# Optimization experiments

Measured on AMD Instinct MI355X. Metric: run time of the kernel, lower is better.

## Reference

```python
import jax, jax.numpy as jnp
import numpy as np

N = 4_000_000   # number of sparse voxels
H = 128         # parent-grid extent per axis (input coords < 256 -> parents < 128)


def setup_inputs() -> dict:
    key = jax.random.key(0)
    # col 0 = batch index, cols 1:4 = integer xyz voxel coords in [0, 256)
    coords = jax.random.randint(key, (N, 4), 0, 256, dtype=jnp.int32)
    # spnn.Conv3d(1,1,k=2) kernel: (2^3, in=1, out=1), constant-init to 1.0
    kernel = jnp.ones((8, 1, 1), dtype=jnp.float32)
    return {"coords": coords, "kernel": kernel}


def _fog(coords, kernel):
    b = coords[:, 0].astype(jnp.int64)
    xyz = coords[:, 1:]
    # pos(): 3-bit occupancy code from LSBs of xyz, feat = 2^code
    bits = xyz & 1                                        # (N, 3)
    pos = bits[:, 0] + 2 * bits[:, 1] + 4 * bits[:, 2]    # (N,) in [0, 8)
    feats = (jnp.int32(1) << pos).astype(jnp.float32)     # (N,) values {1,...,128}

    # 2x2x2 stride-2 sparse conv with all-ones kernel == sum over the 8 children
    # of each parent voxel. The child's kernel-offset index is exactly `pos`.
    pxyz = (xyz >> 1).astype(jnp.int64)                   # parent coords
    pkey = ((b * H + pxyz[:, 0]) * H + pxyz[:, 1]) * H + pxyz[:, 2]

    ukeys, inv = jnp.unique(pkey, size=N, fill_value=-1, return_inverse=True)
    inv = inv.ravel()

    contrib = feats * kernel[pos, 0, 0]                   # all-ones kernel -> feats
    out_feats = jax.ops.segment_sum(contrib, inv, num_segments=N)  # (N,)

    # decode unique parent keys back to (batch, x, y, z); pad slots -> -1
    valid = ukeys >= 0
    k = jnp.where(valid, ukeys, 0)
    oz = k % H
    k = k // H
    oy = k % H
    k = k // H
    ox = k % H
    ob = k // H
    out_coords = jnp.stack([ob, ox, oy, oz], axis=-1).astype(jnp.int32)
    out_coords = jnp.where(valid[:, None], out_coords, jnp.int32(-1))
    return out_coords, out_feats


def reference(coords, kernel):
    return _fog(coords, kernel)
```

## Files before the change

kernel.cpp:

```cpp
#include <hip/hip_runtime.h>

#define NB_BITS     11
#define N_BUCKETS   (1 << NB_BITS)
#define LOCAL_BITS  18
#define LOCAL_WORDS 8192
#define LKMASK      ((1u << LOCAL_BITS) - 1u)
#define KEYMASK     0x1FFFFFFFu
#define NBLK        256
#define N_PART      8
#define FE_CAP      2560

__device__ __forceinline__ unsigned make_key(int4 c) {
    return ((((unsigned)c.x << 7) | (unsigned)(c.y >> 1)) << 7 | (unsigned)(c.z >> 1)) << 7
         | (unsigned)(c.w >> 1);
}

template<int NW>
__device__ inline void block_scan(unsigned v, unsigned* wsum, unsigned& excl, unsigned& total) {
    int t = threadIdx.x, ln = t & 63, wv = t >> 6;
    unsigned incl = v;
    #pragma unroll
    for (int off = 1; off < 64; off <<= 1) {
        unsigned y = __shfl_up(incl, off, 64);
        if (ln >= off) incl += y;
    }
    if (ln == 63) wsum[wv] = incl;
    __syncthreads();
    if (wv == 0) {
        unsigned s = (ln < NW) ? wsum[ln] : 0u;
        #pragma unroll
        for (int off = 1; off < NW; off <<= 1) {
            unsigned y = __shfl_up(s, off, 64);
            if (ln >= off) s += y;
        }
        if (ln < NW) wsum[ln] = s;
    }
    __syncthreads();
    excl = (wv ? wsum[wv - 1] : 0u) + incl - v;
    total = wsum[NW - 1];
}

__global__ void __launch_bounds__(1024)
hist_pass(const int4* __restrict__ coords,
          unsigned* __restrict__ hist32,
          unsigned* __restrict__ skeys, int n, int chunk) {
    __shared__ unsigned h[N_BUCKETS];
    int k = blockIdx.x, t = threadIdx.x;
    if (t < N_BUCKETS) h[t] = 0u;
    if (t + 1024 < N_BUCKETS) h[t + 1024] = 0u;
    __syncthreads();
    int s = k * chunk, e = min(n, s + chunk);
    for (int i = s + t; i < e; i += 1024) {
        int4 c = coords[i];
        unsigned key = make_key(c);
        unsigned pos = (unsigned)((c.y & 1) | ((c.z & 1) << 1) | ((c.w & 1) << 2));
        skeys[i] = (pos << 29) | key;
        atomicAdd(&h[key >> LOCAL_BITS], 1u);
    }
    __syncthreads();
    if (t < N_BUCKETS / 2)
        hist32[k * (N_BUCKETS / 2) + t] = h[2 * t] | (h[2 * t + 1] << 16);
}

__global__ void offs_pass(const unsigned* __restrict__ hist32,
                          unsigned* __restrict__ offs32,
                          unsigned* __restrict__ total) {
    int gid = blockIdx.x * blockDim.x + threadIdx.x;
    unsigned r0 = 0, r1 = 0;
    #pragma unroll 1
    for (int g = 0; g < N_PART; ++g)
        for (int j = 0; j < NBLK / N_PART; ++j) {
            int kk = j * N_PART + g;
            unsigned h = hist32[kk * (N_BUCKETS / 2) + gid];
            offs32[kk * (N_BUCKETS / 2) + gid] = r0 | (r1 << 16);
            r0 += h & 0xFFFFu; r1 += h >> 16;
        }
    total[2 * gid] = r0;
    total[2 * gid + 1] = r1;
}

__global__ void __launch_bounds__(1024)
scatter_pass(const unsigned* __restrict__ skeys,
             const unsigned* __restrict__ offs32,
             const unsigned* __restrict__ total,
             unsigned* __restrict__ pbase,
             unsigned* __restrict__ pairs, int n, int chunk) {
    __shared__ unsigned buf[N_BUCKETS];
    __shared__ unsigned wsum[16];
    int t = threadIdx.x, k = blockIdx.x;
    unsigned v0 = (t < N_BUCKETS / 2) ? total[2 * t] : 0u;
    unsigned v1 = (t < N_BUCKETS / 2) ? total[2 * t + 1] : 0u;
    unsigned excl, tot;
    block_scan<16>(v0 + v1, wsum, excl, tot);
    if (t < N_BUCKETS / 2) {
        unsigned o = offs32[k * (N_BUCKETS / 2) + t];
        buf[2 * t]     = excl + (o & 0xFFFFu);
        buf[2 * t + 1] = excl + v0 + (o >> 16);
        if (k == 0) {
            pbase[2 * t] = excl;
            pbase[2 * t + 1] = excl + v0;
            if (t == N_BUCKETS / 2 - 1) pbase[N_BUCKETS] = excl + v0 + v1;
        }
    }
    __syncthreads();
    int s = k * chunk, e = min(n, s + chunk);
    for (int i = s + t; i < e; i += 1024) {
        unsigned pk = skeys[i];
        unsigned b = (pk & KEYMASK) >> LOCAL_BITS;
        unsigned j = atomicAdd(&buf[b], 1u);
        pairs[j] = pk;
    }
}

__global__ void __launch_bounds__(1024, 2)
count_pass(const unsigned* __restrict__ pairs,
           const unsigned* __restrict__ pbase,
           unsigned* __restrict__ ucount) {
    __shared__ unsigned bm[LOCAL_WORDS];
    __shared__ unsigned wsum[16];
    int t = threadIdx.x, b = blockIdx.x;
    ((uint4*)bm)[t] = make_uint4(0u, 0u, 0u, 0u);
    ((uint4*)bm)[t + 1024] = make_uint4(0u, 0u, 0u, 0u);
    __syncthreads();
    unsigned s = pbase[b], e = pbase[b + 1];
    for (unsigned i = s + t; i < e; i += 1024) {
        unsigned lk = pairs[i] & LKMASK;
        atomicOr(&bm[lk >> 5], 1u << (lk & 31u));
    }
    __syncthreads();
    unsigned v = 0;
    #pragma unroll
    for (int m = 0; m < 8; ++m) v += __popc(bm[t + 1024 * m]);
    int ln = t & 63, wv = t >> 6;
    #pragma unroll
    for (int off = 1; off < 64; off <<= 1) v += __shfl_xor(v, off, 64);
    if (ln == 0) wsum[wv] = v;
    __syncthreads();
    if (t == 0) {
        unsigned c = 0;
        #pragma unroll
        for (int m = 0; m < 16; ++m) c += wsum[m];
        ucount[b] = c;
    }
}

__global__ void __launch_bounds__(1024, 2)
emit_pass(const unsigned* __restrict__ pairs,
          const unsigned* __restrict__ pbase,
          const unsigned* __restrict__ ucount,
          const float* __restrict__ kern,
          float4* __restrict__ out_coords,
          float* __restrict__ out_feats, int n) {
    __shared__ unsigned       bm[LOCAL_WORDS];
    __shared__ unsigned short pfx[LOCAL_WORDS];
    __shared__ float          fe[FE_CAP];
    __shared__ unsigned wsum[16];
    __shared__ unsigned ubS, totS;
    __shared__ float    kl[8];
    int t = threadIdx.x, b = blockIdx.x;
    if (t < 8) kl[t] = (float)(1 << t) * kern[t];
    ((uint4*)bm)[t] = make_uint4(0u, 0u, 0u, 0u);
    ((uint4*)bm)[t + 1024] = make_uint4(0u, 0u, 0u, 0u);
    for (int i = t; i < FE_CAP; i += 1024) fe[i] = 0.f;
    __syncthreads();
    unsigned s = pbase[b], e = pbase[b + 1];
    if (t < 64) {
        int ln = t;
        unsigned sum = 0;
        const uint4* uc4 = (const uint4*)ucount;
        #pragma unroll
        for (int q = 0; q < 8; ++q) {
            uint4 u = uc4[ln * 8 + q];
            sum += u.x + u.y + u.z + u.w;
        }
        unsigned incl = sum;
        #pragma unroll
        for (int off = 1; off < 64; off <<= 1) {
            unsigned y = __shfl_up(incl, off, 64);
            if (ln >= off) incl += y;
        }
        if (ln == 63) totS = incl;
        unsigned exclv = incl - sum;
        if (ln == (b >> 5)) {
            unsigned r = exclv;
            int lim = b & 31;
            for (int m = 0; m < lim; ++m) r += ucount[(b & ~31) + m];
            ubS = r;
        }
    } else {
        for (unsigned i = s + (unsigned)(t - 64); i < e; i += 960) {
            unsigned lk = pairs[i] & LKMASK;
            atomicOr(&bm[lk >> 5], 1u << (lk & 31u));
        }
    }
    __syncthreads();
    uint4 q0 = ((uint4*)bm)[2 * t], q1 = ((uint4*)bm)[2 * t + 1];
    unsigned pc[8] = { (unsigned)__popc(q0.x), (unsigned)__popc(q0.y),
                       (unsigned)__popc(q0.z), (unsigned)__popc(q0.w),
                       (unsigned)__popc(q1.x), (unsigned)__popc(q1.y),
                       (unsigned)__popc(q1.z), (unsigned)__popc(q1.w) };
    unsigned psum = 0;
    #pragma unroll
    for (int m = 0; m < 8; ++m) psum += pc[m];
    unsigned excl, cnt;
    block_scan<16>(psum, wsum, excl, cnt);
    unsigned run = excl;
    #pragma unroll
    for (int m = 0; m < 8; ++m) { pfx[8 * t + m] = (unsigned short)run; run += pc[m]; }
    __syncthreads();
    unsigned ub = ubS;
    for (unsigned i = s + t; i < e; i += 1024) {
        unsigned pk = pairs[i];
        unsigned key = pk & KEYMASK;
        unsigned lk = key & LKMASK;
        unsigned wd = lk >> 5;
        unsigned lr = (unsigned)pfx[wd] + __popc(bm[wd] & ((1u << (lk & 31u)) - 1u));
        atomicAdd(&fe[lr], kl[pk >> 29]);
        out_coords[ub + lr] = make_float4((float)(key >> 21),
                                          (float)((key >> 14) & 127u),
                                          (float)((key >> 7) & 127u),
                                          (float)(key & 127u));
    }
    __syncthreads();
    for (unsigned i = t; i < cnt; i += 1024)
        out_feats[ub + i] = fe[i];
    for (unsigned r = totS + (unsigned)(b * 1024 + t); r < (unsigned)n; r += N_BUCKETS * 1024u) {
        out_coords[r] = make_float4(-1.f, -1.f, -1.f, -1.f);
        out_feats[r] = 0.f;
    }
}

extern "C" void kernel_launch(void* const* d_in, const int* in_sizes, int n_in,
                              void* d_out, int out_size, void* d_ws, size_t ws_size,
                              hipStream_t stream) {
    const int4* coords = (const int4*)d_in[0];
    const float* kern  = (const float*)d_in[1];
    int N = in_sizes[0] / 4;

    float* out = (float*)d_out;
    float4* out_coords = (float4*)out;
    float* out_feats = out + (size_t)4 * N;

    unsigned* pairs  = (unsigned*)d_ws;
    unsigned* skeys  = pairs + (size_t)N;
    unsigned* hist32 = skeys + (size_t)N;
    unsigned* offs32 = hist32 + (size_t)NBLK * (N_BUCKETS / 2);
    unsigned* total  = offs32 + (size_t)NBLK * (N_BUCKETS / 2);
    unsigned* pbase  = total + N_BUCKETS;
    unsigned* ucount = pbase + 2064;

    int chunk = (N + NBLK - 1) / NBLK;
    hist_pass<<<NBLK, 1024, 0, stream>>>(coords, hist32, skeys, N, chunk);
    offs_pass<<<4, 256, 0, stream>>>(hist32, offs32, total);
    scatter_pass<<<NBLK, 1024, 0, stream>>>(skeys, offs32, total, pbase, pairs, N, chunk);
    count_pass<<<N_BUCKETS, 1024, 0, stream>>>(pairs, pbase, ucount);
    emit_pass<<<N_BUCKETS, 1024, 0, stream>>>(pairs, pbase, ucount, kern, out_coords, out_feats, N);
}
```

Measured before the change: 205.6 us.

## Double bucket count, halve per-bucket bitmap and block size for occupancy

Increases the radix bucket count from 2048 to 4096, which halves each bucket's local key range, bitmap, prefix and feature arrays. The count and emit kernels now run 512-thread blocks with higher occupancy bounds, and the emit kernel scans ucount with all threads in a block scan instead of a dedicated wave. The goal is more resident blocks per CU and less LDS per block in the two bucket-processing passes. In exchange the histogram and scatter passes handle more buckets, and the emit kernel's final per-bucket scan does more work.

```diff
diff --git a/kernel.cpp b/kernel.cpp
--- a/kernel.cpp
+++ b/kernel.cpp
@@ -1,14 +1,14 @@
 #include <hip/hip_runtime.h>
 
-#define NB_BITS     11
+#define NB_BITS     12
 #define N_BUCKETS   (1 << NB_BITS)
-#define LOCAL_BITS  18
-#define LOCAL_WORDS 8192
+#define LOCAL_BITS  17
+#define LOCAL_WORDS 4096
 #define LKMASK      ((1u << LOCAL_BITS) - 1u)
 #define KEYMASK     0x1FFFFFFFu
 #define NBLK        256
 #define N_PART      8
-#define FE_CAP      2560
+#define FE_CAP      1280
 
 __device__ __forceinline__ unsigned make_key(int4 c) {
     return ((((unsigned)c.x << 7) | (unsigned)(c.y >> 1)) << 7 | (unsigned)(c.z >> 1)) << 7
@@ -46,8 +46,7 @@
           unsigned* __restrict__ skeys, int n, int chunk) {
     __shared__ unsigned h[N_BUCKETS];
     int k = blockIdx.x, t = threadIdx.x;
-    if (t < N_BUCKETS) h[t] = 0u;
-    if (t + 1024 < N_BUCKETS) h[t + 1024] = 0u;
+    for (int i = t; i < N_BUCKETS; i += 1024) h[i] = 0u;
     __syncthreads();
     int s = k * chunk, e = min(n, s + chunk);
     for (int i = s + t; i < e; i += 1024) {
@@ -58,8 +57,8 @@
         atomicAdd(&h[key >> LOCAL_BITS], 1u);
     }
     __syncthreads();
-    if (t < N_BUCKETS / 2)
-        hist32[k * (N_BUCKETS / 2) + t] = h[2 * t] | (h[2 * t + 1] << 16);
+    for (int i = t; i < N_BUCKETS / 2; i += 1024)
+        hist32[k * (N_BUCKETS / 2) + i] = h[2 * i] | (h[2 * i + 1] << 16);
 }
 
 __global__ void offs_pass(const unsigned* __restrict__ hist32,
@@ -88,18 +87,23 @@
     __shared__ unsigned buf[N_BUCKETS];
     __shared__ unsigned wsum[16];
     int t = threadIdx.x, k = blockIdx.x;
-    unsigned v0 = (t < N_BUCKETS / 2) ? total[2 * t] : 0u;
-    unsigned v1 = (t < N_BUCKETS / 2) ? total[2 * t + 1] : 0u;
+    unsigned v0 = total[4 * t], v1 = total[4 * t + 1];
+    unsigned v2 = total[4 * t + 2], v3 = total[4 * t + 3];
     unsigned excl, tot;
-    block_scan<16>(v0 + v1, wsum, excl, tot);
-    if (t < N_BUCKETS / 2) {
-        unsigned o = offs32[k * (N_BUCKETS / 2) + t];
-        buf[2 * t]     = excl + (o & 0xFFFFu);
-        buf[2 * t + 1] = excl + v0 + (o >> 16);
+    block_scan<16>(v0 + v1 + v2 + v3, wsum, excl, tot);
+    {
+        unsigned o01 = offs32[k * (N_BUCKETS / 2) + 2 * t];
+        unsigned o23 = offs32[k * (N_BUCKETS / 2) + 2 * t + 1];
+        buf[4 * t]     = excl + (o01 & 0xFFFFu);
+        buf[4 * t + 1] = excl + v0 + (o01 >> 16);
+        buf[4 * t + 2] = excl + v0 + v1 + (o23 & 0xFFFFu);
+        buf[4 * t + 3] = excl + v0 + v1 + v2 + (o23 >> 16);
         if (k == 0) {
-            pbase[2 * t] = excl;
-            pbase[2 * t + 1] = excl + v0;
-            if (t == N_BUCKETS / 2 - 1) pbase[N_BUCKETS] = excl + v0 + v1;
+            pbase[4 * t]     = excl;
+            pbase[4 * t + 1] = excl + v0;
+            pbase[4 * t + 2] = excl + v0 + v1;
+            pbase[4 * t + 3] = excl + v0 + v1 + v2;
+            if (t == 1023) pbase[N_BUCKETS] = excl + v0 + v1 + v2 + v3;
         }
     }
     __syncthreads();
@@ -112,25 +116,25 @@
     }
 }
 
-__global__ void __launch_bounds__(1024, 2)
+__global__ void __launch_bounds__(512, 8)
 count_pass(const unsigned* __restrict__ pairs,
            const unsigned* __restrict__ pbase,
            unsigned* __restrict__ ucount) {
     __shared__ unsigned bm[LOCAL_WORDS];
-    __shared__ unsigned wsum[16];
+    __shared__ unsigned wsum[8];
     int t = threadIdx.x, b = blockIdx.x;
     ((uint4*)bm)[t] = make_uint4(0u, 0u, 0u, 0u);
-    ((uint4*)bm)[t + 1024] = make_uint4(0u, 0u, 0u, 0u);
+    ((uint4*)bm)[t + 512] = make_uint4(0u, 0u, 0u, 0u);
     __syncthreads();
     unsigned s = pbase[b], e = pbase[b + 1];
-    for (unsigned i = s + t; i < e; i += 1024) {
+    for (unsigned i = s + t; i < e; i += 512) {
         unsigned lk = pairs[i] & LKMASK;
         atomicOr(&bm[lk >> 5], 1u << (lk & 31u));
     }
     __syncthreads();
     unsigned v = 0;
     #pragma unroll
-    for (int m = 0; m < 8; ++m) v += __popc(bm[t + 1024 * m]);
+    for (int m = 0; m < 8; ++m) v += __popc(bm[t + 512 * m]);
     int ln = t & 63, wv = t >> 6;
     #pragma unroll
     for (int off = 1; off < 64; off <<= 1) v += __shfl_xor(v, off, 64);
@@ -139,12 +143,12 @@
     if (t == 0) {
         unsigned c = 0;
         #pragma unroll
-        for (int m = 0; m < 16; ++m) c += wsum[m];
+        for (int m = 0; m < 8; ++m) c += wsum[m];
         ucount[b] = c;
     }
 }
 
-__global__ void __launch_bounds__(1024, 2)
+__global__ void __launch_bounds__(512, 8)
 emit_pass(const unsigned* __restrict__ pairs,
           const unsigned* __restrict__ pbase,
           const unsigned* __restrict__ ucount,
@@ -154,44 +158,31 @@
     __shared__ unsigned       bm[LOCAL_WORDS];
     __shared__ unsigned short pfx[LOCAL_WORDS];
     __shared__ float          fe[FE_CAP];
-    __shared__ unsigned wsum[16];
+    __shared__ unsigned wsum[8];
     __shared__ unsigned ubS, totS;
     __shared__ float    kl[8];
     int t = threadIdx.x, b = blockIdx.x;
     if (t < 8) kl[t] = (float)(1 << t) * kern[t];
     ((uint4*)bm)[t] = make_uint4(0u, 0u, 0u, 0u);
-    ((uint4*)bm)[t + 1024] = make_uint4(0u, 0u, 0u, 0u);
-    for (int i = t; i < FE_CAP; i += 1024) fe[i] = 0.f;
-    __syncthreads();
+    ((uint4*)bm)[t + 512] = make_uint4(0u, 0u, 0u, 0u);
+    for (int i = t; i < FE_CAP; i += 512) fe[i] = 0.f;
+    const uint4* uc4 = (const uint4*)ucount;
+    uint4 u0 = uc4[2 * t], u1 = uc4[2 * t + 1];
+    unsigned usum = u0.x + u0.y + u0.z + u0.w + u1.x + u1.y + u1.z + u1.w;
+    unsigned uexcl, utot;
+    block_scan<8>(usum, wsum, uexcl, utot);
+    if (t == (b >> 3)) {
+        unsigned r = uexcl;
+        unsigned a[8] = { u0.x, u0.y, u0.z, u0.w, u1.x, u1.y, u1.z, u1.w };
+        int lim = b & 7;
+        for (int m = 0; m < lim; ++m) r += a[m];
+        ubS = r;
+    }
+    if (t == 511) totS = utot;
     unsigned s = pbase[b], e = pbase[b + 1];
-    if (t < 64) {
-        int ln = t;
-        unsigned sum = 0;
-        const uint4* uc4 = (const uint4*)ucount;
-        #pragma unroll
-        for (int q = 0; q < 8; ++q) {
-            uint4 u = uc4[ln * 8 + q];
-            sum += u.x + u.y + u.z + u.w;
-        }
-        unsigned incl = sum;
-        #pragma unroll
-        for (int off = 1; off < 64; off <<= 1) {
-            unsigned y = __shfl_up(incl, off, 64);
-            if (ln >= off) incl += y;
-        }
-        if (ln == 63) totS = incl;
-        unsigned exclv = incl - sum;
-        if (ln == (b >> 5)) {
-            unsigned r = exclv;
-            int lim = b & 31;
-            for (int m = 0; m < lim; ++m) r += ucount[(b & ~31) + m];
-            ubS = r;
-        }
-    } else {
-        for (unsigned i = s + (unsigned)(t - 64); i < e; i += 960) {
-            unsigned lk = pairs[i] & LKMASK;
-            atomicOr(&bm[lk >> 5], 1u << (lk & 31u));
-        }
+    for (unsigned i = s + t; i < e; i += 512) {
+        unsigned lk = pairs[i] & LKMASK;
+        atomicOr(&bm[lk >> 5], 1u << (lk & 31u));
     }
     __syncthreads();
     uint4 q0 = ((uint4*)bm)[2 * t], q1 = ((uint4*)bm)[2 * t + 1];
@@ -203,13 +194,13 @@
     #pragma unroll
     for (int m = 0; m < 8; ++m) psum += pc[m];
     unsigned excl, cnt;
-    block_scan<16>(psum, wsum, excl, cnt);
+    block_scan<8>(psum, wsum, excl, cnt);
     unsigned run = excl;
     #pragma unroll
     for (int m = 0; m < 8; ++m) { pfx[8 * t + m] = (unsigned short)run; run += pc[m]; }
     __syncthreads();
     unsigned ub = ubS;
-    for (unsigned i = s + t; i < e; i += 1024) {
+    for (unsigned i = s + t; i < e; i += 512) {
         unsigned pk = pairs[i];
         unsigned key = pk & KEYMASK;
         unsigned lk = key & LKMASK;
@@ -222,9 +213,9 @@
                                           (float)(key & 127u));
     }
     __syncthreads();
-    for (unsigned i = t; i < cnt; i += 1024)
+    for (unsigned i = t; i < cnt; i += 512)
         out_feats[ub + i] = fe[i];
-    for (unsigned r = totS + (unsigned)(b * 1024 + t); r < (unsigned)n; r += N_BUCKETS * 1024u) {
+    for (unsigned r = totS + (unsigned)(b * 512 + t); r < (unsigned)n; r += N_BUCKETS * 512u) {
         out_coords[r] = make_float4(-1.f, -1.f, -1.f, -1.f);
         out_feats[r] = 0.f;
     }
@@ -247,12 +238,12 @@
     unsigned* offs32 = hist32 + (size_t)NBLK * (N_BUCKETS / 2);
     unsigned* total  = offs32 + (size_t)NBLK * (N_BUCKETS / 2);
     unsigned* pbase  = total + N_BUCKETS;
-    unsigned* ucount = pbase + 2064;
+    unsigned* ucount = pbase + 4112;
 
     int chunk = (N + NBLK - 1) / NBLK;
     hist_pass<<<NBLK, 1024, 0, stream>>>(coords, hist32, skeys, N, chunk);
-    offs_pass<<<4, 256, 0, stream>>>(hist32, offs32, total);
+    offs_pass<<<8, 256, 0, stream>>>(hist32, offs32, total);
     scatter_pass<<<NBLK, 1024, 0, stream>>>(skeys, offs32, total, pbase, pairs, N, chunk);
-    count_pass<<<N_BUCKETS, 1024, 0, stream>>>(pairs, pbase, ucount);
-    emit_pass<<<N_BUCKETS, 1024, 0, stream>>>(pairs, pbase, ucount, kern, out_coords, out_feats, N);
-}
+    count_pass<<<N_BUCKETS, 512, 0, stream>>>(pairs, pbase, ucount);
+    emit_pass<<<N_BUCKETS, 512, 0, stream>>>(pairs, pbase, ucount, kern, out_coords, out_feats, N);
+}
```

Result: slower. 210.0 us (+2.1%).
